# Kernel tuning notes

Hardware: AMD Instinct MI355X
Metric: run time of the kernel (lower is better)

Reference implementation:

```python
import jax, jax.numpy as jnp
import numpy as np

B, L, D, H = 2, 2048, 512, 8
HD = D // H  # head_dim used only for the concat/reshape trick


def setup_inputs() -> dict:
    key = jax.random.key(0)
    ks = jax.random.split(key, 7)
    s = 0.02  # small init so softmax isn't saturated
    return {
        "q": jax.random.normal(ks[0], (B, L, D), jnp.float32),
        "k": jax.random.normal(ks[1], (B, L, D), jnp.float32),
        "v": jax.random.normal(ks[2], (B, L, D), jnp.float32),
        # per-head full-width projections: W[h] is the nn.Linear weight [out,in]
        "Wq": jax.random.normal(ks[3], (H, D, D), jnp.float32) * s,
        "Wk": jax.random.normal(ks[4], (H, D, D), jnp.float32) * s,
        "Wv": jax.random.normal(ks[5], (H, D, D), jnp.float32) * s,
        # output_layer Linear(d_model*num_heads -> d_model, bias=False)
        "Wo": jax.random.normal(ks[6], (D, H * D), jnp.float32) * s,
    }


def reference(q, k, v, Wq, Wk, Wv, Wo):
    # Each head applies its own full d_model x d_model projections (Linear: x @ W^T)
    qh = jnp.einsum('bld,hed->bhle', q, Wq)  # [B,H,L,D]
    kh = jnp.einsum('bld,hed->bhle', k, Wk)
    vh = jnp.einsum('bld,hed->bhle', v, Wv)
    # scaled by sqrt(d_k) with d_k = d_model (as in the original code)
    scores = jnp.einsum('bhle,bhme->bhlm', qh, kh) / jnp.sqrt(jnp.float32(D))
    attn = jax.nn.softmax(scores, axis=-1)          # [B,H,L,L] (dropout = identity in eval)
    ctx = jnp.einsum('bhlm,bhme->bhle', attn, vh)   # [B,H,L,D]
    # torch: each head ctx [B,L,D] -> view(B,L,H,HD); cat over heads on last dim -> [B,L,H,H*HD]; flatten
    comb = ctx.reshape(B, H, L, H, HD).transpose(0, 2, 3, 1, 4).reshape(B, L, H * D)
    out = comb @ Wo.T                               # [B,L,D]
    return out, attn
```

## Files before the change

kernel.cpp:

```cpp
#include <hip/hip_runtime.h>
#include <cstdio>
#include <cstdint>


#define AS1 __attribute__((address_space(1)))
#define AS3 __attribute__((address_space(3)))

typedef __attribute__((ext_vector_type(8))) short bf16x8;
typedef __attribute__((ext_vector_type(4))) short short4v;
typedef __attribute__((ext_vector_type(4))) float f32x4;
typedef __attribute__((ext_vector_type(4))) _Float16 h4;

constexpr int cB = 2, cH = 8, cL = 2048, cD = 512;
constexpr float SCORE_SCALE = 0.044194173824159216f;

__device__ __forceinline__ short f2bf(float f) {
  return __builtin_bit_cast(short, static_cast<__bf16>(f));
}

__device__ __forceinline__ void gload16(const void* g, void* l) {
  __builtin_amdgcn_global_load_lds((AS1 const void*)g, (AS3 void*)l, 16, 0, 0);
}

struct CvtArgs { const float4* s[7]; short4v* d[7]; };

__global__ __launch_bounds__(256) void cvt_all(CvtArgs a) {
  const int z = blockIdx.y;
  const int i = blockIdx.x * 256 + threadIdx.x;
  const float4 v = a.s[z][i];
  short4v o = { f2bf(v.x), f2bf(v.y), f2bf(v.z), f2bf(v.w) };
  a.d[z][i] = o;
}

enum { M_PROJ = 0, M_PROJV = 1, M_SCORES = 2, M_OUT = 3 };

template <int MODE>
__global__ __launch_bounds__(256) void gemm_nt(const short* __restrict__ Ap,
                                               const short* __restrict__ Bp,
                                               void* __restrict__ Cp,
                                               float2* __restrict__ Sp) {
  constexpr int K   = (MODE == M_OUT) ? 1024 : 512;
  constexpr int LDA = (MODE == M_OUT) ? 4096 : 512;
  constexpr int LDB = (MODE == M_OUT) ? 4096 : 512;

  __shared__ short As[3][128 * 32];
  __shared__ short Bs[3][128 * 32];

  const int t = threadIdx.x;
  const int lane = t & 63;
  const int wv = t >> 6;
  const int wm = wv >> 1, wn = wv & 1;
  const int z = blockIdx.z;

  size_t Aoff, Boff;
  if constexpr (MODE == M_PROJ || MODE == M_PROJV) {
    Aoff = (size_t)(z >> 3) * ((size_t)cL * cD);
    Boff = (size_t)(z & 7) * ((size_t)cD * cD);
  } else if constexpr (MODE == M_SCORES) {
    Aoff = (size_t)z * ((size_t)cL * cD);
    Boff = (size_t)z * ((size_t)cL * cD);
  } else {
    Aoff = (size_t)(z >> 2) * ((size_t)cL * 4096) + (size_t)(z & 3) * 1024;
    Boff = (size_t)(z & 3) * 1024;
  }

  const short* Ag0 = Ap + Aoff + (size_t)(blockIdx.y * 128) * LDA;
  const short* Bg0 = Bp + Boff + (size_t)(blockIdx.x * 128) * LDB;

  f32x4 acc[4][4];
#pragma unroll
  for (int i = 0; i < 4; ++i)
#pragma unroll
    for (int j = 0; j < 4; ++j) acc[i][j] = (f32x4){0.f, 0.f, 0.f, 0.f};

  auto stage = [&](int b, int kt) {
#pragma unroll
    for (int r = 0; r < 2; ++r) {
      const int cbase = r * 256 + wv * 64;
      const int c = cbase + lane;
      const int row = c >> 2, col = (c & 3) * 8;
      gload16(Ag0 + (size_t)row * LDA + kt + col, &As[b][cbase * 8]);
    }
#pragma unroll
    for (int r = 0; r < 2; ++r) {
      const int cbase = r * 256 + wv * 64;
      const int c = cbase + lane;
      const int row = c >> 2, col = (c & 3) * 8;
      gload16(Bg0 + (size_t)row * LDB + kt + col, &Bs[b][cbase * 8]);
    }
  };

  const int koff = (lane >> 4) * 8;
  const int ar = wm * 64 + (lane & 15);
  const int br = wn * 64 + (lane & 15);

  constexpr int nt = K / 32;
  stage(0, 0);
  stage(1, 32);
  int cur = 0, pre = 2;
  for (int tt = 0; tt < nt; ++tt) {
    if (tt < nt - 1) { asm volatile("s_waitcnt vmcnt(4) lgkmcnt(0)" ::: "memory"); }
    else             { asm volatile("s_waitcnt vmcnt(0) lgkmcnt(0)" ::: "memory"); }
    __builtin_amdgcn_sched_barrier(0);
    __builtin_amdgcn_s_barrier();
    __builtin_amdgcn_sched_barrier(0);
    if (tt + 2 < nt) stage(pre, (tt + 2) * 32);
    __builtin_amdgcn_sched_barrier(0);

    bf16x8 af[4], bfv[4];
#pragma unroll
    for (int i = 0; i < 4; ++i) af[i] = *(const bf16x8*)&As[cur][(ar + i * 16) * 32 + koff];
#pragma unroll
    for (int j = 0; j < 4; ++j) bfv[j] = *(const bf16x8*)&Bs[cur][(br + j * 16) * 32 + koff];
    __builtin_amdgcn_s_setprio(1);
#pragma unroll
    for (int i = 0; i < 4; ++i)
#pragma unroll
      for (int j = 0; j < 4; ++j)
        acc[i][j] = __builtin_amdgcn_mfma_f32_16x16x32_bf16(af[i], bfv[j], acc[i][j], 0, 0, 0);
    __builtin_amdgcn_s_setprio(0);
    cur = (cur == 2) ? 0 : cur + 1;
    pre = (pre == 2) ? 0 : pre + 1;
  }

  const int r0 = (lane >> 4) * 4;
  const int cc = lane & 15;
  const int rowbase = blockIdx.y * 128 + wm * 64 + r0;
  const int colbase = blockIdx.x * 128 + wn * 64 + cc;

  if constexpr (MODE == M_PROJ) {
    short* C = (short*)Cp + (size_t)z * ((size_t)cL * cD);
#pragma unroll
    for (int i = 0; i < 4; ++i)
#pragma unroll
      for (int j = 0; j < 4; ++j)
#pragma unroll
        for (int r = 0; r < 4; ++r)
          C[(size_t)(rowbase + i * 16 + r) * cD + (colbase + j * 16)] = f2bf(acc[i][j][r]);
  } else if constexpr (MODE == M_PROJV) {
    short* C = (short*)Cp + (size_t)z * ((size_t)cD * cL);
#pragma unroll
    for (int i = 0; i < 4; ++i)
#pragma unroll
      for (int j = 0; j < 4; ++j) {
        short4v o = { f2bf(acc[i][j][0]), f2bf(acc[i][j][1]),
                      f2bf(acc[i][j][2]), f2bf(acc[i][j][3]) };
        *(short4v*)&C[(size_t)(colbase + j * 16) * cL + (rowbase + i * 16)] = o;
      }
  } else if constexpr (MODE == M_SCORES) {
    char* Cb = (char*)Cp + ((size_t)z << 24);
    float2* ps = Sp + (size_t)z * ((size_t)cL * 32);
    const int pid = blockIdx.x * 2 + wn;
#pragma unroll
    for (int i = 0; i < 4; ++i) {
      float sv[4][4];
#pragma unroll
      for (int j = 0; j < 4; ++j)
#pragma unroll
        for (int r = 0; r < 4; ++r) sv[j][r] = acc[i][j][r] * SCORE_SCALE;
#pragma unroll
      for (int j = 0; j < 4; ++j)
#pragma unroll
        for (int r = 0; r < 4; ++r) {
          const _Float16 hv = (_Float16)sv[j][r];
          __builtin_nontemporal_store(
              __builtin_bit_cast(short, hv),
              (short*)(Cb + (size_t)(rowbase + i * 16 + r) * 8192 + 4096 +
                       (size_t)(colbase + j * 16) * 2));
        }
#pragma unroll
      for (int r = 0; r < 4; ++r) {
        float mx = fmaxf(fmaxf(sv[0][r], sv[1][r]), fmaxf(sv[2][r], sv[3][r]));
#pragma unroll
        for (int off = 1; off < 16; off <<= 1) mx = fmaxf(mx, __shfl_xor(mx, off, 64));
        float sm = __expf(sv[0][r] - mx) + __expf(sv[1][r] - mx) +
                   __expf(sv[2][r] - mx) + __expf(sv[3][r] - mx);
#pragma unroll
        for (int off = 1; off < 16; off <<= 1) sm += __shfl_xor(sm, off, 64);
        if ((lane & 15) == 0)
          ps[(size_t)(rowbase + i * 16 + r) * 32 + pid] = make_float2(mx, sm);
      }
    }
  } else {
    float* C = (float*)Cp + (size_t)((z & 3) * 2 + (z >> 2)) * ((size_t)cL * cD);
#pragma unroll
    for (int i = 0; i < 4; ++i)
#pragma unroll
      for (int j = 0; j < 4; ++j)
#pragma unroll
        for (int r = 0; r < 4; ++r)
          C[(size_t)(rowbase + i * 16 + r) * cD + (colbase + j * 16)] = acc[i][j][r];
  }
}

__global__ __launch_bounds__(512, 4) void fused_ctx(const short* __restrict__ vhT,
                                                    const float2* __restrict__ pstats,
                                                    float* __restrict__ attn,
                                                    short* __restrict__ comb) {
  __shared__ short Bs[2][512 * 32];
  __shared__ short Pb[2][64 * 32];

  const int t = threadIdx.x;
  const int lane = t & 63;
  const int wv = t >> 6;
  const int rowblk = blockIdx.x;
  const int z = blockIdx.y;

  const int trow = t >> 3;
  const int tcb = t & 7;
  const int pidx = trow * 32 + (((tcb >> 1) ^ ((trow >> 1) & 3)) << 3) + ((tcb & 1) << 2);
  const int grow = rowblk * 64 + trow;

  const float2* pp = pstats + ((size_t)z * cL + grow) * 32 + tcb * 4;
  const float2 q0 = pp[0], q1 = pp[1], q2 = pp[2], q3 = pp[3];
  float m = fmaxf(fmaxf(q0.x, q1.x), fmaxf(q2.x, q3.x));
#pragma unroll
  for (int off = 1; off < 8; off <<= 1) m = fmaxf(m, __shfl_xor(m, off, 64));
  float l = q0.y * __expf(q0.x - m) + q1.y * __expf(q1.x - m) +
            q2.y * __expf(q2.x - m) + q3.y * __expf(q3.x - m);
#pragma unroll
  for (int off = 1; off < 8; off <<= 1) l += __shfl_xor(l, off, 64);
  const float invl = 1.0f / l;

  char* rowb = (char*)attn + ((size_t)z << 24) + (size_t)grow * 8192;
  float* spf = (float*)rowb + tcb * 4;
  const h4* sph = (const h4*)(rowb + 4096);

  const short* Bg = vhT + (size_t)z * ((size_t)cD * cL);

  f32x4 acc[4][4];
#pragma unroll
  for (int i = 0; i < 4; ++i)
#pragma unroll
    for (int j = 0; j < 4; ++j) acc[i][j] = (f32x4){0.f, 0.f, 0.f, 0.f};

  const int qk = lane >> 4;
  const int arr = lane & 15;
  const int br = wv * 64 + (lane & 15);

  auto stageB = [&](int nb, int kt) {
#pragma unroll
    for (int r = 0; r < 4; ++r) {
      const int cbase = r * 512 + wv * 64;
      const int c = cbase + lane;
      const int row = c >> 2;
      const int swcol = ((c & 3) ^ ((row >> 1) & 3)) * 8;
      gload16(Bg + (size_t)row * cL + kt + swcol, &Bs[nb][cbase * 8]);
    }
  };
  auto transform = [&](int ck, h4 hv) -> short4v {
    const float p0 = __expf((float)hv[0] - m) * invl;
    const float p1 = __expf((float)hv[1] - m) * invl;
    const float p2 = __expf((float)hv[2] - m) * invl;
    const float p3 = __expf((float)hv[3] - m) * invl;
    __builtin_nontemporal_store((f32x4){p0, p1, p2, p3}, (f32x4*)(spf + ck * 32));
    short4v pb = { f2bf(p0), f2bf(p1), f2bf(p2), f2bf(p3) };
    return pb;
  };

  stageB(0, 0);
  h4 hc = __builtin_nontemporal_load(sph + tcb);
  short4v pb = transform(0, hc);
  hc = __builtin_nontemporal_load(sph + tcb + 8);
  *(short4v*)&Pb[0][pidx] = pb;

  for (int k = 0; k < 63; ++k) {
    const int cb = k & 1, nb = cb ^ 1;
    pb = transform(k + 1, hc);
    const int kc = (k + 2) & 63;
    hc = __builtin_nontemporal_load(sph + tcb + kc * 8);
    asm volatile("s_waitcnt vmcnt(2) lgkmcnt(0)" ::: "memory");
    __builtin_amdgcn_sched_barrier(0);
    __builtin_amdgcn_s_barrier();
    __builtin_amdgcn_sched_barrier(0);
    *(short4v*)&Pb[nb][pidx] = pb;
    stageB(nb, (k + 1) * 32);
    __builtin_amdgcn_sched_barrier(0);
    bf16x8 af[4], bfv[4];
#pragma unroll
    for (int i = 0; i < 4; ++i) {
      const int rA = arr + i * 16;
      af[i] = *(const bf16x8*)&Pb[cb][rA * 32 + ((qk ^ ((rA >> 1) & 3)) << 3)];
    }
#pragma unroll
    for (int j = 0; j < 4; ++j) {
      const int rB = br + j * 16;
      bfv[j] = *(const bf16x8*)&Bs[cb][rB * 32 + ((qk ^ ((rB >> 1) & 3)) << 3)];
    }
    __builtin_amdgcn_s_setprio(1);
#pragma unroll
    for (int i = 0; i < 4; ++i)
#pragma unroll
      for (int j = 0; j < 4; ++j)
        acc[i][j] = __builtin_amdgcn_mfma_f32_16x16x32_bf16(af[i], bfv[j], acc[i][j], 0, 0, 0);
    __builtin_amdgcn_s_setprio(0);
  }

  asm volatile("s_waitcnt vmcnt(0) lgkmcnt(0)" ::: "memory");
  __builtin_amdgcn_sched_barrier(0);
  __builtin_amdgcn_s_barrier();
  __builtin_amdgcn_sched_barrier(0);
  {
    bf16x8 af[4], bfv[4];
#pragma unroll
    for (int i = 0; i < 4; ++i) {
      const int rA = arr + i * 16;
      af[i] = *(const bf16x8*)&Pb[1][rA * 32 + ((qk ^ ((rA >> 1) & 3)) << 3)];
    }
#pragma unroll
    for (int j = 0; j < 4; ++j) {
      const int rB = br + j * 16;
      bfv[j] = *(const bf16x8*)&Bs[1][rB * 32 + ((qk ^ ((rB >> 1) & 3)) << 3)];
    }
    __builtin_amdgcn_s_setprio(1);
#pragma unroll
    for (int i = 0; i < 4; ++i)
#pragma unroll
      for (int j = 0; j < 4; ++j)
        acc[i][j] = __builtin_amdgcn_mfma_f32_16x16x32_bf16(af[i], bfv[j], acc[i][j], 0, 0, 0);
    __builtin_amdgcn_s_setprio(0);
  }

  const int r0 = (lane >> 4) * 4;
  const int cc = lane & 15;
  short* C = comb + (size_t)(z >> 3) * ((size_t)cL * (cH * cD));
  const int h = z & 7;
  const int rowbase = rowblk * 64 + r0;
#pragma unroll
  for (int i = 0; i < 4; ++i)
#pragma unroll
    for (int j = 0; j < 4; ++j) {
      const int e = wv * 64 + j * 16 + cc;
      const int jc = ((e >> 6) << 9) + (h << 6) + (e & 63);
#pragma unroll
      for (int r = 0; r < 4; ++r)
        C[(size_t)(rowbase + i * 16 + r) * (cH * cD) + jc] = f2bf(acc[i][j][r]);
    }
}

__global__ __launch_bounds__(256) void add_quads(const float* __restrict__ p,
                                                 float* __restrict__ out) {
  const int i = blockIdx.x * 256 + threadIdx.x;
  constexpr int S = cB * cL * cD;
  const f32x4 a = __builtin_nontemporal_load((const f32x4*)p + i);
  const f32x4 b = __builtin_nontemporal_load((const f32x4*)(p + S) + i);
  const f32x4 c = __builtin_nontemporal_load((const f32x4*)(p + 2 * S) + i);
  const f32x4 d = __builtin_nontemporal_load((const f32x4*)(p + 3 * S) + i);
  const f32x4 s = a + b + c + d;
  *((f32x4*)out + i) = s;
}

extern "C" void kernel_launch(void* const* d_in, const int* in_sizes, int n_in,
                              void* d_out, int out_size, void* d_ws, size_t ws_size,
                              hipStream_t stream) {
  (void)in_sizes; (void)n_in; (void)out_size;

  const float* q  = (const float*)d_in[0];
  const float* k  = (const float*)d_in[1];
  const float* v  = (const float*)d_in[2];
  const float* Wq = (const float*)d_in[3];
  const float* Wk = (const float*)d_in[4];
  const float* Wv = (const float*)d_in[5];
  const float* Wo = (const float*)d_in[6];

  float* out  = (float*)d_out;
  float* attn = out + (size_t)cB * cL * cD;

  constexpr size_t Mi = 1ull << 20;
  char* ws = (char*)d_ws;
  short* qbf = (short*)(ws + 0 * Mi);
  short* kbf = (short*)(ws + 4 * Mi);
  short* vbf = (short*)(ws + 8 * Mi);
  short* wqb = (short*)(ws + 12 * Mi);
  short* wkb = (short*)(ws + 16 * Mi);
  short* wvb = (short*)(ws + 20 * Mi);
  short* wob = (short*)(ws + 24 * Mi);
  short* qh  = (short*)(ws + 28 * Mi);
  short* kh  = (short*)(ws + 60 * Mi);
  short* vhT = (short*)(ws + 92 * Mi);
  short* comb = qh;
  float2* pstats = (float2*)(ws + 4 * Mi);
  float*  pout   = (float*)(ws + 60 * Mi);

  if (ws_size < 124 * Mi) {
    fprintf(stderr, "kernel_launch: ws too small (%zu < %zu)\n", ws_size, 124 * Mi);
    return;
  }

  CvtArgs ca;
  ca.s[0] = (const float4*)q;  ca.d[0] = (short4v*)qbf;
  ca.s[1] = (const float4*)k;  ca.d[1] = (short4v*)kbf;
  ca.s[2] = (const float4*)v;  ca.d[2] = (short4v*)vbf;
  ca.s[3] = (const float4*)Wq; ca.d[3] = (short4v*)wqb;
  ca.s[4] = (const float4*)Wk; ca.d[4] = (short4v*)wkb;
  ca.s[5] = (const float4*)Wv; ca.d[5] = (short4v*)wvb;
  ca.s[6] = (const float4*)Wo; ca.d[6] = (short4v*)wob;
  cvt_all<<<dim3(2048, 7), 256, 0, stream>>>(ca);

  gemm_nt<M_PROJ ><<<dim3(4, 16, 16), 256, 0, stream>>>(qbf, wqb, qh, nullptr);
  gemm_nt<M_PROJ ><<<dim3(4, 16, 16), 256, 0, stream>>>(kbf, wkb, kh, nullptr);
  gemm_nt<M_PROJV><<<dim3(4, 16, 16), 256, 0, stream>>>(vbf, wvb, vhT, nullptr);

  gemm_nt<M_SCORES><<<dim3(16, 16, 16), 256, 0, stream>>>(qh, kh, attn, pstats);

  fused_ctx<<<dim3(32, cB * cH), 512, 0, stream>>>(vhT, pstats, attn, comb);

  gemm_nt<M_OUT><<<dim3(4, 16, 8), 256, 0, stream>>>(comb, wob, (void*)pout, nullptr);

  add_quads<<<2048, 256, 0, stream>>>(pout, out);
}
```

Before: 709.6 us.

## Remap block indices for XCD-aware L2 locality and drop nontemporal hints

Block indices in the GEMMs and the fused context kernel are remapped so that consecutive hardware-dispatched blocks (round-robined across the 8 XCDs) which share the same batch-head land on the same XCD. The goal is more L2 reuse of shared operands within each XCD. The fp16 score stores and loads also switch from nontemporal to regular accesses, so the score matrix written by the scores kernel can stay in cache for the context kernel. The cost is a little index arithmetic per block and possible cache pollution from the large score writes.

```diff
diff --git a/kernel.cpp b/kernel.cpp
--- a/kernel.cpp
+++ b/kernel.cpp
@@ -43,6 +43,17 @@
   constexpr int LDA = (MODE == M_OUT) ? 4096 : 512;
   constexpr int LDB = (MODE == M_OUT) ? 4096 : 512;
 
+  constexpr int GX  = (MODE == M_SCORES) ? 16 : 4;
+  constexpr int GY  = 16;
+  constexpr int GZ  = (MODE == M_OUT) ? 8 : 16;
+  constexpr int ZPX = GZ / 8;
+  constexpr int GXY = GX * GY;
+  const int li = (int)blockIdx.z * GXY + (int)blockIdx.y * GX + (int)blockIdx.x;
+  const int sfl = li >> 3;
+  const int bz = (li & 7) * ZPX + sfl / GXY;
+  const int rem = sfl % GXY;
+  const int by = rem / GX, bx = rem % GX;
+
   __shared__ short As[3][128 * 32];
   __shared__ short Bs[3][128 * 32];
 
@@ -50,22 +61,21 @@
   const int lane = t & 63;
   const int wv = t >> 6;
   const int wm = wv >> 1, wn = wv & 1;
-  const int z = blockIdx.z;
 
   size_t Aoff, Boff;
   if constexpr (MODE == M_PROJ || MODE == M_PROJV) {
-    Aoff = (size_t)(z >> 3) * ((size_t)cL * cD);
-    Boff = (size_t)(z & 7) * ((size_t)cD * cD);
+    Aoff = (size_t)(bz >> 3) * ((size_t)cL * cD);
+    Boff = (size_t)(bz & 7) * ((size_t)cD * cD);
   } else if constexpr (MODE == M_SCORES) {
-    Aoff = (size_t)z * ((size_t)cL * cD);
-    Boff = (size_t)z * ((size_t)cL * cD);
+    Aoff = (size_t)bz * ((size_t)cL * cD);
+    Boff = (size_t)bz * ((size_t)cL * cD);
   } else {
-    Aoff = (size_t)(z >> 2) * ((size_t)cL * 4096) + (size_t)(z & 3) * 1024;
-    Boff = (size_t)(z & 3) * 1024;
-  }
-
-  const short* Ag0 = Ap + Aoff + (size_t)(blockIdx.y * 128) * LDA;
-  const short* Bg0 = Bp + Boff + (size_t)(blockIdx.x * 128) * LDB;
+    Aoff = (size_t)(bz >> 2) * ((size_t)cL * 4096) + (size_t)(bz & 3) * 1024;
+    Boff = (size_t)(bz & 3) * 1024;
+  }
+
+  const short* Ag0 = Ap + Aoff + (size_t)(by * 128) * LDA;
+  const short* Bg0 = Bp + Boff + (size_t)(bx * 128) * LDB;
 
   f32x4 acc[4][4];
 #pragma unroll
@@ -125,11 +135,11 @@
 
   const int r0 = (lane >> 4) * 4;
   const int cc = lane & 15;
-  const int rowbase = blockIdx.y * 128 + wm * 64 + r0;
-  const int colbase = blockIdx.x * 128 + wn * 64 + cc;
+  const int rowbase = by * 128 + wm * 64 + r0;
+  const int colbase = bx * 128 + wn * 64 + cc;
 
   if constexpr (MODE == M_PROJ) {
-    short* C = (short*)Cp + (size_t)z * ((size_t)cL * cD);
+    short* C = (short*)Cp + (size_t)bz * ((size_t)cL * cD);
 #pragma unroll
     for (int i = 0; i < 4; ++i)
 #pragma unroll
@@ -138,7 +148,7 @@
         for (int r = 0; r < 4; ++r)
           C[(size_t)(rowbase + i * 16 + r) * cD + (colbase + j * 16)] = f2bf(acc[i][j][r]);
   } else if constexpr (MODE == M_PROJV) {
-    short* C = (short*)Cp + (size_t)z * ((size_t)cD * cL);
+    short* C = (short*)Cp + (size_t)bz * ((size_t)cD * cL);
 #pragma unroll
     for (int i = 0; i < 4; ++i)
 #pragma unroll
@@ -148,9 +158,9 @@
         *(short4v*)&C[(size_t)(colbase + j * 16) * cL + (rowbase + i * 16)] = o;
       }
   } else if constexpr (MODE == M_SCORES) {
-    char* Cb = (char*)Cp + ((size_t)z << 24);
-    float2* ps = Sp + (size_t)z * ((size_t)cL * 32);
-    const int pid = blockIdx.x * 2 + wn;
+    char* Cb = (char*)Cp + ((size_t)bz << 24);
+    float2* ps = Sp + (size_t)bz * ((size_t)cL * 32);
+    const int pid = bx * 2 + wn;
 #pragma unroll
     for (int i = 0; i < 4; ++i) {
       float sv[4][4];
@@ -163,10 +173,8 @@
 #pragma unroll
         for (int r = 0; r < 4; ++r) {
           const _Float16 hv = (_Float16)sv[j][r];
-          __builtin_nontemporal_store(
-              __builtin_bit_cast(short, hv),
-              (short*)(Cb + (size_t)(rowbase + i * 16 + r) * 8192 + 4096 +
-                       (size_t)(colbase + j * 16) * 2));
+          *(short*)(Cb + (size_t)(rowbase + i * 16 + r) * 8192 + 4096 +
+                    (size_t)(colbase + j * 16) * 2) = __builtin_bit_cast(short, hv);
         }
 #pragma unroll
       for (int r = 0; r < 4; ++r) {
@@ -182,7 +190,7 @@
       }
     }
   } else {
-    float* C = (float*)Cp + (size_t)((z & 3) * 2 + (z >> 2)) * ((size_t)cL * cD);
+    float* C = (float*)Cp + (size_t)((bz & 3) * 2 + (bz >> 2)) * ((size_t)cL * cD);
 #pragma unroll
     for (int i = 0; i < 4; ++i)
 #pragma unroll
@@ -203,8 +211,10 @@
   const int t = threadIdx.x;
   const int lane = t & 63;
   const int wv = t >> 6;
-  const int rowblk = blockIdx.x;
-  const int z = blockIdx.y;
+  const int li = blockIdx.x;
+  const int sfl = li >> 3;
+  const int z = (li & 7) * 2 + (sfl >> 5);
+  const int rowblk = sfl & 31;
 
   const int trow = t >> 3;
   const int tcb = t & 7;
@@ -259,16 +269,16 @@
   };
 
   stageB(0, 0);
-  h4 hc = __builtin_nontemporal_load(sph + tcb);
+  h4 hc = sph[tcb];
   short4v pb = transform(0, hc);
-  hc = __builtin_nontemporal_load(sph + tcb + 8);
+  hc = sph[tcb + 8];
   *(short4v*)&Pb[0][pidx] = pb;
 
   for (int k = 0; k < 63; ++k) {
     const int cb = k & 1, nb = cb ^ 1;
     pb = transform(k + 1, hc);
     const int kc = (k + 2) & 63;
-    hc = __builtin_nontemporal_load(sph + tcb + kc * 8);
+    hc = sph[tcb + kc * 8];
     asm volatile("s_waitcnt vmcnt(2) lgkmcnt(0)" ::: "memory");
     __builtin_amdgcn_sched_barrier(0);
     __builtin_amdgcn_s_barrier();
@@ -403,7 +413,7 @@
 
   gemm_nt<M_SCORES><<<dim3(16, 16, 16), 256, 0, stream>>>(qh, kh, attn, pstats);
 
-  fused_ctx<<<dim3(32, cB * cH), 512, 0, stream>>>(vhT, pstats, attn, comb);
+  fused_ctx<<<dim3(512), 512, 0, stream>>>(vhT, pstats, attn, comb);
 
   gemm_nt<M_OUT><<<dim3(4, 16, 8), 256, 0, stream>>>(comb, wob, (void*)pout, nullptr);
 
```

Result: faster. 677.4 us (-4.5%).
